# Kernel optimization log

Hardware: AMD Instinct MI355X
Metric: run time of the kernel (lower is better)

The kernel has to match this reference:

```python
import jax, jax.numpy as jnp
import numpy as np

ACT_BITS = 8
QMAX = float(2 ** ACT_BITS - 1)  # unsigned fake-quant range [0, 255]


def setup_inputs() -> dict:
    key = jax.random.key(0)
    k_x, k_w, k_b = jax.random.split(key, 3)
    B, S, D_IN, D_OUT = 4, 2048, 4096, 4096
    x = jax.random.normal(k_x, (B, S, D_IN), dtype=jnp.float32)
    # per-tensor int-quantized weight [out_features, in_features]
    qweight = jax.random.randint(k_w, (D_OUT, D_IN), 0, 256, dtype=jnp.int32)
    scale = jnp.asarray(0.01, dtype=jnp.float32)
    zero_point = jnp.asarray(128, dtype=jnp.int32)
    bias = jax.random.normal(k_b, (D_OUT,), dtype=jnp.float32) * 0.02
    act_scale = jnp.asarray(0.02, dtype=jnp.float32)
    act_zero_point = jnp.asarray(128, dtype=jnp.int32)
    return {
        "x": x,
        "qweight": qweight,
        "scale": scale,
        "zero_point": zero_point,
        "bias": bias,
        "act_scale": act_scale,
        "act_zero_point": act_zero_point,
    }


def reference(x, qweight, scale, zero_point, bias, act_scale, act_zero_point):
    # --- activation fake-quant (quantize then dequantize, per-tensor) ---
    azp = act_zero_point.astype(jnp.float32)
    x_q = jnp.clip(jnp.round(x / act_scale) + azp, 0.0, QMAX)
    x_fq = (x_q - azp) * act_scale
    # --- weight dequant: (q - zp) * scale, per-tensor scalar params ---
    w = (qweight.astype(jnp.float32) - zero_point.astype(jnp.float32)) * scale
    # --- dense GEMM: F.linear(x, w, bias) = x @ w.T + bias ---
    return jnp.einsum("bsd,od->bso", x_fq, w) + bias
```

## Files before the change

kernel.cpp:

```cpp
#include <hip/hip_runtime.h>
#include <hip/hip_bf16.h>


typedef __attribute__((ext_vector_type(4))) int   int4v;
typedef __attribute__((ext_vector_type(4))) float f32x4;

#define TILE 128
#define BK 64

__global__ __launch_bounds__(256) void quant_x_kernel(
    const float* __restrict__ x, int* __restrict__ xq,
    const float* __restrict__ act_scale_p, const int* __restrict__ act_zp_p,
    int n16)
{
    int g = blockIdx.x * blockDim.x + threadIdx.x;
    if (g >= n16) return;
    const float s   = act_scale_p[0];
    const float azp = (float)act_zp_p[0];
    const float lo = -azp, hi = 255.0f - azp;
    const float4* xin = (const float4*)x + (size_t)g * 4;
    int4v out;
#pragma unroll
    for (int w = 0; w < 4; w++) {
        float4 v = xin[w];
        float f0 = fminf(fmaxf(rintf(v.x / s), lo), hi);
        float f1 = fminf(fmaxf(rintf(v.y / s), lo), hi);
        float f2 = fminf(fmaxf(rintf(v.z / s), lo), hi);
        float f3 = fminf(fmaxf(rintf(v.w / s), lo), hi);
        unsigned int b0 = (unsigned int)(int)f0 & 0xff;
        unsigned int b1 = (unsigned int)(int)f1 & 0xff;
        unsigned int b2 = (unsigned int)(int)f2 & 0xff;
        unsigned int b3 = (unsigned int)(int)f3 & 0xff;
        out[w] = (int)(b0 | (b1 << 8) | (b2 << 16) | (b3 << 24));
    }
    ((int4v*)xq)[g] = out;
}

__global__ __launch_bounds__(256) void quant_w_kernel(
    const int* __restrict__ qw, int* __restrict__ wq,
    const int* __restrict__ zp_p, int n16)
{
    int g = blockIdx.x * blockDim.x + threadIdx.x;
    if (g >= n16) return;
    const int zp = zp_p[0];
    const int4* win = (const int4*)qw + (size_t)g * 4;
    int4v out;
#pragma unroll
    for (int w = 0; w < 4; w++) {
        int4 v = win[w];
        unsigned int b0 = (unsigned int)(v.x - zp) & 0xff;
        unsigned int b1 = (unsigned int)(v.y - zp) & 0xff;
        unsigned int b2 = (unsigned int)(v.z - zp) & 0xff;
        unsigned int b3 = (unsigned int)(v.w - zp) & 0xff;
        out[w] = (int)(b0 | (b1 << 8) | (b2 << 16) | (b3 << 24));
    }
    ((int4v*)wq)[g] = out;
}

#define ASYNC_CP16(gp, lp)                                                      \
    __builtin_amdgcn_global_load_lds(                                           \
        (const __attribute__((address_space(1))) unsigned int*)(gp),            \
        (__attribute__((address_space(3))) unsigned int*)(lp), 16, 0, 0)

__global__ __launch_bounds__(256) void gemm_i8_kernel(
    const signed char* __restrict__ A,
    const signed char* __restrict__ B,
    const float* __restrict__ bias,
    const float* __restrict__ scale_p, const float* __restrict__ act_scale_p,
    float* __restrict__ C, int M, int N, int K)
{
    __shared__ __align__(16) signed char As[TILE * BK];
    __shared__ __align__(16) signed char Bs[TILE * BK];

    const int tid  = threadIdx.x;
    const int lane = tid & 63;
    const int wave = tid >> 6;
    const int bm = blockIdx.y * TILE;
    const int bn = blockIdx.x * TILE;

    const int srow = tid >> 2;
    const int scol = (((tid & 3) ^ ((tid >> 3) & 3)) * 16);
    const signed char* a_ptr0 = A + (size_t)(bm + srow)      * K + scol;
    const signed char* a_ptr1 = A + (size_t)(bm + srow + 64) * K + scol;
    const signed char* b_ptr0 = B + (size_t)(bn + srow)      * K + scol;
    const signed char* b_ptr1 = B + (size_t)(bn + srow + 64) * K + scol;
    signed char* as0 = &As[(size_t)tid * 16];
    signed char* as1 = &As[(size_t)(tid + 256) * 16];
    signed char* bs0 = &Bs[(size_t)tid * 16];
    signed char* bs1 = &Bs[(size_t)(tid + 256) * 16];

    const int wm = (wave >> 1) * 64;
    const int wn = (wave & 1) * 64;
    const int fr = lane & 15;
    const int koff = (((lane >> 4) ^ ((lane >> 1) & 3)) * 16);

    int4v acc[4][4] = {};

    for (int k0 = 0; k0 < K; k0 += BK) {
        ASYNC_CP16(a_ptr0, as0);
        ASYNC_CP16(a_ptr1, as1);
        ASYNC_CP16(b_ptr0, bs0);
        ASYNC_CP16(b_ptr1, bs1);
        a_ptr0 += BK; a_ptr1 += BK; b_ptr0 += BK; b_ptr1 += BK;
        __syncthreads();

        int4v af[4], bf[4];
#pragma unroll
        for (int i = 0; i < 4; i++)
            af[i] = *(const int4v*)&As[(wm + i * 16 + fr) * BK + koff];
#pragma unroll
        for (int j = 0; j < 4; j++)
            bf[j] = *(const int4v*)&Bs[(wn + j * 16 + fr) * BK + koff];
#pragma unroll
        for (int i = 0; i < 4; i++)
#pragma unroll
            for (int j = 0; j < 4; j++)
                acc[i][j] = __builtin_amdgcn_mfma_i32_16x16x64_i8(
                    af[i], bf[j], acc[i][j], 0, 0, 0);
        __syncthreads();
    }

    const float sc = scale_p[0] * act_scale_p[0];
    const int crow = (lane >> 4) * 4;
    const int ccol = lane & 15;
#pragma unroll
    for (int i = 0; i < 4; i++) {
        const int m = bm + wm + i * 16 + crow;
#pragma unroll
        for (int j = 0; j < 4; j++) {
            const int n = bn + wn + j * 16 + ccol;
            const float bv = bias[n];
#pragma unroll
            for (int r = 0; r < 4; r++) {
                C[(size_t)(m + r) * N + n] = (float)acc[i][j][r] * sc + bv;
            }
        }
    }
}

extern "C" void kernel_launch(void* const* d_in, const int* in_sizes, int n_in,
                              void* d_out, int out_size, void* d_ws, size_t ws_size,
                              hipStream_t stream) {
    const float* x         = (const float*)d_in[0];
    const int*   qw        = (const int*)  d_in[1];
    const float* scale     = (const float*)d_in[2];
    const int*   zp        = (const int*)  d_in[3];
    const float* bias      = (const float*)d_in[4];
    const float* act_scale = (const float*)d_in[5];
    const int*   act_zp    = (const int*)  d_in[6];
    float* out = (float*)d_out;

    const int D_OUT = in_sizes[4];
    const int D_IN  = in_sizes[1] / D_OUT;
    const int M = in_sizes[0] / D_IN;
    const int N = D_OUT, K = D_IN;

    signed char* xq = (signed char*)d_ws;
    signed char* wq = xq + (size_t)M * K;

    const int n16x = (M * K) / 16;
    quant_x_kernel<<<(n16x + 255) / 256, 256, 0, stream>>>(x, (int*)xq, act_scale, act_zp, n16x);

    const int n16w = (N * K) / 16;
    quant_w_kernel<<<(n16w + 255) / 256, 256, 0, stream>>>(qw, (int*)wq, zp, n16w);

    dim3 grid(N / TILE, M / TILE);
    gemm_i8_kernel<<<grid, 256, 0, stream>>>(xq, wq, bias, scale, act_scale,
                                             out, M, N, K);
}
```

Baseline: 443.1 us.

## Enlarge int8 GEMM tile to 256x128x128 and simplify quant kernels

The GEMM tile grows from 128x128 with BK=64 to 256x128 with BK=128. Each wave now computes a 64x128 sub-tile (4x8 MFMAs), with a new 8-way XOR swizzle for LDS and two k-substeps per barrier. This cuts global reloads per output and halves the number of barrier pairs along K. The cost is 48KB of LDS per block and many more accumulator registers, which can lower occupancy. The quantize kernels now process 4 elements per thread instead of 16, so they launch more threads, each doing less work.

```diff
diff --git a/kernel.cpp b/kernel.cpp
--- a/kernel.cpp
+++ b/kernel.cpp
@@ -2,59 +2,47 @@
 #include <hip/hip_bf16.h>
 
 
-typedef __attribute__((ext_vector_type(4))) int   int4v;
-typedef __attribute__((ext_vector_type(4))) float f32x4;
+typedef __attribute__((ext_vector_type(4))) int int4v;
 
-#define TILE 128
-#define BK 64
+#define BM 256
+#define BN 128
+#define BK 128
 
 __global__ __launch_bounds__(256) void quant_x_kernel(
-    const float* __restrict__ x, int* __restrict__ xq,
+    const float4* __restrict__ x, unsigned int* __restrict__ xq,
     const float* __restrict__ act_scale_p, const int* __restrict__ act_zp_p,
-    int n16)
+    int n4)
 {
     int g = blockIdx.x * blockDim.x + threadIdx.x;
-    if (g >= n16) return;
+    if (g >= n4) return;
     const float s   = act_scale_p[0];
     const float azp = (float)act_zp_p[0];
     const float lo = -azp, hi = 255.0f - azp;
-    const float4* xin = (const float4*)x + (size_t)g * 4;
-    int4v out;
-#pragma unroll
-    for (int w = 0; w < 4; w++) {
-        float4 v = xin[w];
-        float f0 = fminf(fmaxf(rintf(v.x / s), lo), hi);
-        float f1 = fminf(fmaxf(rintf(v.y / s), lo), hi);
-        float f2 = fminf(fmaxf(rintf(v.z / s), lo), hi);
-        float f3 = fminf(fmaxf(rintf(v.w / s), lo), hi);
-        unsigned int b0 = (unsigned int)(int)f0 & 0xff;
-        unsigned int b1 = (unsigned int)(int)f1 & 0xff;
-        unsigned int b2 = (unsigned int)(int)f2 & 0xff;
-        unsigned int b3 = (unsigned int)(int)f3 & 0xff;
-        out[w] = (int)(b0 | (b1 << 8) | (b2 << 16) | (b3 << 24));
-    }
-    ((int4v*)xq)[g] = out;
+    float4 v = x[g];
+    float f0 = fminf(fmaxf(rintf(v.x / s), lo), hi);
+    float f1 = fminf(fmaxf(rintf(v.y / s), lo), hi);
+    float f2 = fminf(fmaxf(rintf(v.z / s), lo), hi);
+    float f3 = fminf(fmaxf(rintf(v.w / s), lo), hi);
+    unsigned int b0 = (unsigned int)(int)f0 & 0xff;
+    unsigned int b1 = (unsigned int)(int)f1 & 0xff;
+    unsigned int b2 = (unsigned int)(int)f2 & 0xff;
+    unsigned int b3 = (unsigned int)(int)f3 & 0xff;
+    xq[g] = b0 | (b1 << 8) | (b2 << 16) | (b3 << 24);
 }
 
 __global__ __launch_bounds__(256) void quant_w_kernel(
-    const int* __restrict__ qw, int* __restrict__ wq,
-    const int* __restrict__ zp_p, int n16)
+    const int4* __restrict__ qw, unsigned int* __restrict__ wq,
+    const int* __restrict__ zp_p, int n4)
 {
     int g = blockIdx.x * blockDim.x + threadIdx.x;
-    if (g >= n16) return;
+    if (g >= n4) return;
     const int zp = zp_p[0];
-    const int4* win = (const int4*)qw + (size_t)g * 4;
-    int4v out;
-#pragma unroll
-    for (int w = 0; w < 4; w++) {
-        int4 v = win[w];
-        unsigned int b0 = (unsigned int)(v.x - zp) & 0xff;
-        unsigned int b1 = (unsigned int)(v.y - zp) & 0xff;
-        unsigned int b2 = (unsigned int)(v.z - zp) & 0xff;
-        unsigned int b3 = (unsigned int)(v.w - zp) & 0xff;
-        out[w] = (int)(b0 | (b1 << 8) | (b2 << 16) | (b3 << 24));
-    }
-    ((int4v*)wq)[g] = out;
+    int4 v = qw[g];
+    unsigned int b0 = (unsigned int)(v.x - zp) & 0xff;
+    unsigned int b1 = (unsigned int)(v.y - zp) & 0xff;
+    unsigned int b2 = (unsigned int)(v.z - zp) & 0xff;
+    unsigned int b3 = (unsigned int)(v.w - zp) & 0xff;
+    wq[g] = b0 | (b1 << 8) | (b2 << 16) | (b3 << 24);
 }
 
 #define ASYNC_CP16(gp, lp)                                                      \
@@ -62,61 +50,63 @@
         (const __attribute__((address_space(1))) unsigned int*)(gp),            \
         (__attribute__((address_space(3))) unsigned int*)(lp), 16, 0, 0)
 
-__global__ __launch_bounds__(256) void gemm_i8_kernel(
+__global__ __launch_bounds__(256, 2) void gemm_i8_kernel(
     const signed char* __restrict__ A,
     const signed char* __restrict__ B,
     const float* __restrict__ bias,
     const float* __restrict__ scale_p, const float* __restrict__ act_scale_p,
     float* __restrict__ C, int M, int N, int K)
 {
-    __shared__ __align__(16) signed char As[TILE * BK];
-    __shared__ __align__(16) signed char Bs[TILE * BK];
+    __shared__ __align__(16) signed char As[BM * BK];
+    __shared__ __align__(16) signed char Bs[BN * BK];
 
     const int tid  = threadIdx.x;
     const int lane = tid & 63;
     const int wave = tid >> 6;
-    const int bm = blockIdx.y * TILE;
-    const int bn = blockIdx.x * TILE;
+    const int bm = blockIdx.y * BM;
+    const int bn = blockIdx.x * BN;
 
-    const int srow = tid >> 2;
-    const int scol = (((tid & 3) ^ ((tid >> 3) & 3)) * 16);
-    const signed char* a_ptr0 = A + (size_t)(bm + srow)      * K + scol;
-    const signed char* a_ptr1 = A + (size_t)(bm + srow + 64) * K + scol;
-    const signed char* b_ptr0 = B + (size_t)(bn + srow)      * K + scol;
-    const signed char* b_ptr1 = B + (size_t)(bn + srow + 64) * K + scol;
-    signed char* as0 = &As[(size_t)tid * 16];
-    signed char* as1 = &As[(size_t)(tid + 256) * 16];
-    signed char* bs0 = &Bs[(size_t)tid * 16];
-    signed char* bs1 = &Bs[(size_t)(tid + 256) * 16];
+    const int srow = tid >> 3;
+    const int scol = ((tid & 7) ^ (srow & 7)) * 16;
+    const signed char* aP = A + (size_t)(bm + srow) * K + scol;
+    const signed char* bP = B + (size_t)(bn + srow) * K + scol;
+    signed char* asD = &As[(size_t)tid * 16];
+    signed char* bsD = &Bs[(size_t)tid * 16];
 
-    const int wm = (wave >> 1) * 64;
-    const int wn = (wave & 1) * 64;
+    const int wm = wave * 64;
     const int fr = lane & 15;
-    const int koff = (((lane >> 4) ^ ((lane >> 1) & 3)) * 16);
+    const int g4 = lane >> 4;
+    const int x7 = fr & 7;
 
-    int4v acc[4][4] = {};
+    int4v acc[4][8] = {};
 
     for (int k0 = 0; k0 < K; k0 += BK) {
-        ASYNC_CP16(a_ptr0, as0);
-        ASYNC_CP16(a_ptr1, as1);
-        ASYNC_CP16(b_ptr0, bs0);
-        ASYNC_CP16(b_ptr1, bs1);
-        a_ptr0 += BK; a_ptr1 += BK; b_ptr0 += BK; b_ptr1 += BK;
+#pragma unroll
+        for (int r = 0; r < 8; r++)
+            ASYNC_CP16(aP + (size_t)r * 32 * K, asD + r * 4096);
+#pragma unroll
+        for (int r = 0; r < 4; r++)
+            ASYNC_CP16(bP + (size_t)r * 32 * K, bsD + r * 4096);
+        aP += BK; bP += BK;
         __syncthreads();
 
-        int4v af[4], bf[4];
 #pragma unroll
-        for (int i = 0; i < 4; i++)
-            af[i] = *(const int4v*)&As[(wm + i * 16 + fr) * BK + koff];
+        for (int kk = 0; kk < 2; kk++) {
+            const int ko = ((kk * 4 + g4) ^ x7) * 16;
+            int4v af[4], bf[8];
 #pragma unroll
-        for (int j = 0; j < 4; j++)
-            bf[j] = *(const int4v*)&Bs[(wn + j * 16 + fr) * BK + koff];
+            for (int i = 0; i < 4; i++)
+                af[i] = *(const int4v*)&As[(wm + i * 16 + fr) * BK + ko];
 #pragma unroll
-        for (int i = 0; i < 4; i++)
+            for (int j = 0; j < 8; j++)
+                bf[j] = *(const int4v*)&Bs[(j * 16 + fr) * BK + ko];
 #pragma unroll
-            for (int j = 0; j < 4; j++)
-                acc[i][j] = __builtin_amdgcn_mfma_i32_16x16x64_i8(
-                    af[i], bf[j], acc[i][j], 0, 0, 0);
+            for (int i = 0; i < 4; i++)
+#pragma unroll
+                for (int j = 0; j < 8; j++)
+                    acc[i][j] = __builtin_amdgcn_mfma_i32_16x16x64_i8(
+                        af[i], bf[j], acc[i][j], 0, 0, 0);
+        }
         __syncthreads();
     }
 
@@ -127,8 +117,8 @@
     for (int i = 0; i < 4; i++) {
         const int m = bm + wm + i * 16 + crow;
 #pragma unroll
-        for (int j = 0; j < 4; j++) {
-            const int n = bn + wn + j * 16 + ccol;
+        for (int j = 0; j < 8; j++) {
+            const int n = bn + j * 16 + ccol;
             const float bv = bias[n];
 #pragma unroll
             for (int r = 0; r < 4; r++) {
@@ -158,13 +148,15 @@
     signed char* xq = (signed char*)d_ws;
     signed char* wq = xq + (size_t)M * K;
 
-    const int n16x = (M * K) / 16;
-    quant_x_kernel<<<(n16x + 255) / 256, 256, 0, stream>>>(x, (int*)xq, act_scale, act_zp, n16x);
+    const int n4x = (M * K) / 4;
+    quant_x_kernel<<<(n4x + 255) / 256, 256, 0, stream>>>(
+        (const float4*)x, (unsigned int*)xq, act_scale, act_zp, n4x);
 
-    const int n16w = (N * K) / 16;
-    quant_w_kernel<<<(n16w + 255) / 256, 256, 0, stream>>>(qw, (int*)wq, zp, n16w);
+    const int n4w = (N * K) / 4;
+    quant_w_kernel<<<(n4w + 255) / 256, 256, 0, stream>>>(
+        (const int4*)qw, (unsigned int*)wq, zp, n4w);
 
-    dim3 grid(N / TILE, M / TILE);
+    dim3 grid(N / BN, M / BM);
     gemm_i8_kernel<<<grid, 256, 0, stream>>>(xq, wq, bias, scale, act_scale,
                                              out, M, N, K);
 }
```

Result: faster. 381.1 us (-14.0%).
